# Performance work log

Hardware: AMD Instinct MI355X
Metric: run time of the kernel (lower is better)

Reference implementation:

```python
import math
import jax, jax.numpy as jnp
import numpy as np

B, C, HH, WW = 1, 256, 64, 64
NUM_HEADS = 8
GROUPS = 8
EPS = 1e-5


def setup_inputs() -> dict:
    key = jax.random.key(0)
    ks = jax.random.split(key, 5)
    x = jax.random.normal(ks[0], (B, C, HH, WW), dtype=jnp.float32)
    gn_gamma = jnp.ones((C,), dtype=jnp.float32)
    gn_beta = jnp.zeros((C,), dtype=jnp.float32)
    qkv_w = jax.random.normal(ks[1], (3 * C, C), dtype=jnp.float32) / math.sqrt(C)
    qkv_b = jax.random.normal(ks[2], (3 * C,), dtype=jnp.float32) * 0.02
    proj_w = jax.random.normal(ks[3], (C, C), dtype=jnp.float32) / math.sqrt(C)
    proj_b = jax.random.normal(ks[4], (C,), dtype=jnp.float32) * 0.02
    return {"x": x, "gn_gamma": gn_gamma, "gn_beta": gn_beta,
            "qkv_w": qkv_w, "qkv_b": qkv_b, "proj_w": proj_w, "proj_b": proj_b}


def reference(x, gn_gamma, gn_beta, qkv_w, qkv_b, proj_w, proj_b):
    b, c, h, w = x.shape
    t = h * w
    xf = x.reshape(b, c, t)
    # GroupNorm(8, C): normalize over (C/8 channels x T spatial) per group
    xg = xf.reshape(b, GROUPS, (c // GROUPS) * t)
    mean = xg.mean(axis=-1, keepdims=True)
    var = xg.var(axis=-1, keepdims=True)
    xn = ((xg - mean) * jax.lax.rsqrt(var + EPS)).reshape(b, c, t)
    xn = xn * gn_gamma[:, None] + gn_beta[:, None]
    # 1x1 Conv1d C -> 3C is a channel matmul
    qkv = jnp.einsum('oc,bct->bot', qkv_w, xn) + qkv_b[:, None]  # [b, 3C, t]
    nh = NUM_HEADS
    ch = c // nh
    q, k, v = jnp.split(qkv, 3, axis=1)  # each [b, C, t]
    q = q.reshape(b * nh, ch, t)
    k = k.reshape(b * nh, ch, t)
    v = v.reshape(b * nh, ch, t)
    scale = 1.0 / math.sqrt(math.sqrt(ch))
    weight = jnp.einsum('bct,bcs->bts', q * scale, k * scale)  # [b*nh, t, t]
    weight = jax.nn.softmax(weight.astype(jnp.float32), axis=-1).astype(qkv.dtype)
    a = jnp.einsum('bts,bcs->bct', weight, v).reshape(b, c, t)
    hout = jnp.einsum('oc,bct->bot', proj_w, a) + proj_b[:, None]
    return x + hout.reshape(b, c, h, w)
```

## Files before the change

### kernel.cpp

```cpp
#include <hip/hip_runtime.h>
#include <hip/hip_bf16.h>
#include <math.h>

#define C_DIM 256
#define T_DIM 4096
#define NHEADS 8
#define NGROUPS 8
#define NSPLIT 4
#define SRANGE (T_DIM / NSPLIT)
#define NT (SRANGE / 64)

typedef __attribute__((ext_vector_type(8))) short bf16x8;
typedef __attribute__((ext_vector_type(4))) float f32x4;

#if __has_builtin(__builtin_amdgcn_exp2f)
#define EXP2(x) __builtin_amdgcn_exp2f(x)
#else
#define EXP2(x) exp2f(x)
#endif

#define MFMA16(a, b, c) __builtin_amdgcn_mfma_f32_16x16x32_bf16(a, b, c, 0, 0, 0)

#define WS_PSUM 0
#define WS_PSQ  256
#define WS_QT_F   1024
#define WS_KT_F   (WS_QT_F + 524288)
#define WS_VB_F   (WS_KT_F + 524288)
#define WS_WQB_F  (WS_VB_F + 524288)
#define WS_WPB_F  (WS_WQB_F + 98304)
#define WS_OP_F   (WS_WPB_F + 32768)
#define WS_L_F    (WS_OP_F + NSPLIT * 256 * 4096 / 2)

#define QSCALE 0.2550348527f

__device__ __forceinline__ ushort f2bf(float f) {
  union { float f; unsigned u; } v; v.f = f;
  return (ushort)((v.u + 0x7fffu + ((v.u >> 16) & 1u)) >> 16);
}

__device__ __forceinline__ float bf2f(ushort u) {
  union { unsigned u; float f; } v; v.u = ((unsigned)u) << 16;
  return v.f;
}

__device__ __forceinline__ uint pk2(float a, float b) {
  __hip_bfloat162 h = __float22bfloat162_rn(make_float2(a, b));
  union { __hip_bfloat162 h; uint u; } c; c.h = h; return c.u;
}

__global__ __launch_bounds__(256) void prep(const float* __restrict__ x,
                                            const float* __restrict__ wq,
                                            const float* __restrict__ wp,
                                            float* __restrict__ ws,
                                            ushort* __restrict__ wqb,
                                            ushort* __restrict__ wpb) {
  const int i4 = (blockIdx.x * 256 + threadIdx.x) * 4;
  const int n1 = 768 * 256;
  if (i4 < n1) {
    float4 v = *(const float4*)(wq + i4);
    union { ushort us[4]; uint2 u; } pk;
    pk.us[0] = f2bf(v.x); pk.us[1] = f2bf(v.y); pk.us[2] = f2bf(v.z); pk.us[3] = f2bf(v.w);
    *(uint2*)(wqb + i4) = pk.u;
  } else {
    const int j = i4 - n1;
    float4 v = *(const float4*)(wp + j);
    union { ushort us[4]; uint2 u; } pk;
    pk.us[0] = f2bf(v.x); pk.us[1] = f2bf(v.y); pk.us[2] = f2bf(v.z); pk.us[3] = f2bf(v.w);
    *(uint2*)(wpb + j) = pk.u;
  }
  const int g = blockIdx.x >> 5;
  const int bx = blockIdx.x & 31;
  const size_t base = (size_t)g * 131072 + (size_t)bx * 4096;
  float s = 0.f, s2 = 0.f;
  for (int i = threadIdx.x; i < 4096; i += 256) {
    float v = x[base + i];
    s += v;
    s2 += v * v;
  }
#pragma unroll
  for (int mask = 1; mask <= 32; mask <<= 1) {
    s += __shfl_xor(s, mask, 64);
    s2 += __shfl_xor(s2, mask, 64);
  }
  __shared__ float red[8];
  const int wid = threadIdx.x >> 6;
  if ((threadIdx.x & 63) == 0) { red[wid] = s; red[4 + wid] = s2; }
  __syncthreads();
  if (threadIdx.x == 0) {
    ws[WS_PSUM + g * 32 + bx] = red[0] + red[1] + red[2] + red[3];
    ws[WS_PSQ + g * 32 + bx] = red[4] + red[5] + red[6] + red[7];
  }
}

__global__ __launch_bounds__(256) void qkv_mfma(const float* __restrict__ x,
                                                const float* __restrict__ gamma,
                                                const float* __restrict__ beta,
                                                const float* __restrict__ ws,
                                                const ushort* __restrict__ wqb,
                                                const float* __restrict__ bias,
                                                ushort* __restrict__ qt,
                                                ushort* __restrict__ kt,
                                                ushort* __restrict__ vb) {
  const int t0 = blockIdx.x * 16;
  const int oc = blockIdx.y;
  __shared__ ushort A[16 * 256];
  __shared__ float fg[256], fb[256];
  __shared__ float sm_stat[16];
  const int tid = threadIdx.x;
  {
    const int gg = tid >> 5, i = tid & 31;
    float s = ws[WS_PSUM + gg * 32 + i];
    float s2 = ws[WS_PSQ + gg * 32 + i];
#pragma unroll
    for (int mask = 1; mask <= 16; mask <<= 1) {
      s += __shfl_xor(s, mask, 32);
      s2 += __shfl_xor(s2, mask, 32);
    }
    if (i == 0) {
      const float inv_n = 1.0f / 131072.0f;
      float mean = s * inv_n;
      float var = s2 * inv_n - mean * mean;
      sm_stat[gg] = mean;
      sm_stat[8 + gg] = rsqrtf(var + 1e-5f);
    }
  }
  __syncthreads();
  {
    const int c = tid, gg = c >> 5;
    float fgv = gamma[c] * sm_stat[8 + gg];
    fg[c] = fgv; fb[c] = beta[c] - sm_stat[gg] * fgv;
  }
  __syncthreads();
#pragma unroll
  for (int p = 0; p < 4; ++p) {
    const int idx = p * 256 + tid;
    const int c = idx >> 2;
    const int tin = (idx & 3) * 4;
    float4 xv = *(const float4*)(x + (size_t)c * T_DIM + t0 + tin);
    const float fgc = fg[c], fbc = fb[c];
    float xn[4] = {fmaf(xv.x, fgc, fbc), fmaf(xv.y, fgc, fbc),
                   fmaf(xv.z, fgc, fbc), fmaf(xv.w, fgc, fbc)};
#pragma unroll
    for (int i = 0; i < 4; ++i) {
      const int t = tin + i;
      A[t * 256 + (c ^ ((t & 7) << 3))] = f2bf(xn[i]);
    }
  }
  __syncthreads();

  const int w = tid >> 6, lane = tid & 63, l15 = lane & 15, g = lane >> 4;
  const int o_loc = w * 64;
  f32x4 acc[4] = {};
  const ushort* wrow[4];
#pragma unroll
  for (int j = 0; j < 4; ++j)
    wrow[j] = wqb + (size_t)(oc * 256 + o_loc + j * 16 + l15) * 256;

  bf16x8 bc[4], bn[4];
#pragma unroll
  for (int j = 0; j < 4; ++j) bc[j] = *(const bf16x8*)(wrow[j] + 8 * g);

#pragma unroll
  for (int kk = 0; kk < 8; ++kk) {
    const bf16x8 af = *(const bf16x8*)(&A[l15 * 256 + ((kk * 32 + 8 * g) ^ ((l15 & 7) << 3))]);
    if (kk < 7) {
#pragma unroll
      for (int j = 0; j < 4; ++j) bn[j] = *(const bf16x8*)(wrow[j] + (kk + 1) * 32 + 8 * g);
    }
#pragma unroll
    for (int j = 0; j < 4; ++j)
      acc[j] = MFMA16(af, bc[j], acc[j]);
#pragma unroll
    for (int j = 0; j < 4; ++j) bc[j] = bn[j];
  }

  if (oc == 2) {
#pragma unroll
    for (int j = 0; j < 4; ++j) {
      const int o = o_loc + j * 16 + l15;
      const float bo = bias[512 + o];
      union { ushort us[4]; uint2 u; } pk;
#pragma unroll
      for (int r = 0; r < 4; ++r) pk.us[r] = f2bf(acc[j][r] + bo);
      *(uint2*)(vb + (size_t)o * T_DIM + t0 + 4 * g) = pk.u;
    }
  } else {
    const float scale = (oc == 0) ? QSCALE : 1.0f;
    __syncthreads();
#pragma unroll
    for (int j = 0; j < 4; ++j) {
      const int o = o_loc + j * 16 + l15;
      const float bo = bias[oc * 256 + o];
#pragma unroll
      for (int r = 0; r < 4; ++r) {
        const int t = 4 * g + r;
        A[t * 256 + (o ^ ((t & 7) << 3))] = f2bf((acc[j][r] + bo) * scale);
      }
    }
    __syncthreads();
    ushort* dst = (oc == 0) ? qt : kt;
    const int hh = tid >> 5;
    const int tt = (tid >> 1) & 15;
    const int d0 = (tid & 1) * 16;
    const int sw = (tt & 7) << 3;
    uint4 v0 = *(uint4*)&A[tt * 256 + ((hh * 32 + d0) ^ sw)];
    uint4 v1 = *(uint4*)&A[tt * 256 + ((hh * 32 + d0 + 8) ^ sw)];
    ushort* gp = dst + ((size_t)hh * T_DIM + t0 + tt) * 32 + d0;
    *(uint4*)gp = v0;
    *(uint4*)(gp + 8) = v1;
  }
}

__global__ __launch_bounds__(256, 4) void attn_fwd(const ushort* __restrict__ qt,
                                                   const ushort* __restrict__ kt,
                                                   const ushort* __restrict__ vb,
                                                   ushort* __restrict__ Op,
                                                   float* __restrict__ Lb) {
  const int bid = blockIdx.x;
  const int h = bid & 7;
  const int inner = bid >> 3;
  const int qb = inner & 31;
  const int z = inner >> 5;
  const int tid = threadIdx.x;
  const int w = tid >> 6, lane = tid & 63, l15 = lane & 15, g = lane >> 4;

  __shared__ ushort Klds[2][64 * 40];
  __shared__ ushort Vlds[2][32 * 72];

  const int t_a = qb * 128 + w * 16 + l15;
  const int t_b = t_a + 64;
  const bf16x8 qfa = *(const bf16x8*)(qt + ((size_t)(h * T_DIM + t_a) * 32 + 8 * g));
  const bf16x8 qfb = *(const bf16x8*)(qt + ((size_t)(h * T_DIM + t_b) * 32 + 8 * g));

  f32x4 Oa0 = {}, Oa1 = {}, Ob0 = {}, Ob1 = {};
  float la = 0.f, lb = 0.f;

  const int sbeg = z * SRANGE;
  const int p_row = tid >> 2;
  const int q5 = p_row & 31;
  const int sm_row = (p_row & 32) + 16 * ((q5 >> 2) & 1) + 4 * (q5 >> 3) + (q5 & 3);
  const ushort* kgp = kt + (size_t)h * T_DIM * 32 + (size_t)(sbeg + p_row) * 32 + (tid & 3) * 8;
  const ushort* vgp = vb + (size_t)(h * 32 + (tid >> 3)) * T_DIM + sbeg + (tid & 7) * 8;
  ushort* kw0 = &Klds[0][sm_row * 40 + (tid & 3) * 8];
  ushort* vw0 = &Vlds[0][(tid >> 3) * 72 + (tid & 7) * 8];
  {
    *(uint4*)kw0 = *(const uint4*)kgp;
    *(uint4*)vw0 = *(const uint4*)vgp;
  }
  uint4 kn = *(const uint4*)(kgp + 2048);
  uint4 vn = *(const uint4*)(vgp + 64);
  __syncthreads();

  int cur = 0;
  for (int t = 0; t < NT; ++t) {
    if (t + 1 < NT) {
      *(uint4*)(kw0 + (cur ^ 1) * (64 * 40)) = kn;
      *(uint4*)(vw0 + (cur ^ 1) * (32 * 72)) = vn;
      if (t + 2 < NT) {
        kn = *(const uint4*)(kgp + (size_t)(t + 2) * 2048);
        vn = *(const uint4*)(vgp + (t + 2) * 64);
      }
    }

    const ushort* kbase = &Klds[cur][0];
    const ushort* vbase = &Vlds[cur][0];
    const f32x4 z4 = {};
    const bf16x8 kf0 = *(const bf16x8*)(kbase + (0 * 16 + l15) * 40 + 8 * g);
    const bf16x8 kf1 = *(const bf16x8*)(kbase + (1 * 16 + l15) * 40 + 8 * g);
    const bf16x8 kf2 = *(const bf16x8*)(kbase + (2 * 16 + l15) * 40 + 8 * g);
    const bf16x8 kf3 = *(const bf16x8*)(kbase + (3 * 16 + l15) * 40 + 8 * g);
    __builtin_amdgcn_s_setprio(1);
    f32x4 sa0 = MFMA16(kf0, qfa, z4);
    f32x4 sa1 = MFMA16(kf1, qfa, z4);
    f32x4 sa2 = MFMA16(kf2, qfa, z4);
    f32x4 sa3 = MFMA16(kf3, qfa, z4);
    f32x4 sb0 = MFMA16(kf0, qfb, z4);
    f32x4 sb1 = MFMA16(kf1, qfb, z4);
    f32x4 sb2 = MFMA16(kf2, qfb, z4);
    f32x4 sb3 = MFMA16(kf3, qfb, z4);
    __builtin_amdgcn_s_setprio(0);

    const bf16x8 vf00 = *(const bf16x8*)(vbase + (l15) * 72 + 8 * g);
    const bf16x8 vf01 = *(const bf16x8*)(vbase + (l15) * 72 + 32 + 8 * g);
    const bf16x8 vf10 = *(const bf16x8*)(vbase + (16 + l15) * 72 + 8 * g);
    const bf16x8 vf11 = *(const bf16x8*)(vbase + (16 + l15) * 72 + 32 + 8 * g);

    union { uint u[4]; bf16x8 v; } fa0, fa1, fb0, fb1;
    {
      float p0, p1, p2, p3, p4, p5, p6, p7;
      p0 = EXP2(sa0[0]); p1 = EXP2(sa0[1]); p2 = EXP2(sa0[2]); p3 = EXP2(sa0[3]);
      p4 = EXP2(sa1[0]); p5 = EXP2(sa1[1]); p6 = EXP2(sa1[2]); p7 = EXP2(sa1[3]);
      la += ((p0 + p1) + (p2 + p3)) + ((p4 + p5) + (p6 + p7));
      fa0.u[0] = pk2(p0, p1); fa0.u[1] = pk2(p2, p3);
      fa0.u[2] = pk2(p4, p5); fa0.u[3] = pk2(p6, p7);
      p0 = EXP2(sa2[0]); p1 = EXP2(sa2[1]); p2 = EXP2(sa2[2]); p3 = EXP2(sa2[3]);
      p4 = EXP2(sa3[0]); p5 = EXP2(sa3[1]); p6 = EXP2(sa3[2]); p7 = EXP2(sa3[3]);
      la += ((p0 + p1) + (p2 + p3)) + ((p4 + p5) + (p6 + p7));
      fa1.u[0] = pk2(p0, p1); fa1.u[1] = pk2(p2, p3);
      fa1.u[2] = pk2(p4, p5); fa1.u[3] = pk2(p6, p7);
    }

    __builtin_amdgcn_s_setprio(1);
    Oa0 = MFMA16(vf00, fa0.v, Oa0);
    Oa0 = MFMA16(vf01, fa1.v, Oa0);
    Oa1 = MFMA16(vf10, fa0.v, Oa1);
    Oa1 = MFMA16(vf11, fa1.v, Oa1);
    __builtin_amdgcn_s_setprio(0);

    {
      float p0, p1, p2, p3, p4, p5, p6, p7;
      p0 = EXP2(sb0[0]); p1 = EXP2(sb0[1]); p2 = EXP2(sb0[2]); p3 = EXP2(sb0[3]);
      p4 = EXP2(sb1[0]); p5 = EXP2(sb1[1]); p6 = EXP2(sb1[2]); p7 = EXP2(sb1[3]);
      lb += ((p0 + p1) + (p2 + p3)) + ((p4 + p5) + (p6 + p7));
      fb0.u[0] = pk2(p0, p1); fb0.u[1] = pk2(p2, p3);
      fb0.u[2] = pk2(p4, p5); fb0.u[3] = pk2(p6, p7);
      p0 = EXP2(sb2[0]); p1 = EXP2(sb2[1]); p2 = EXP2(sb2[2]); p3 = EXP2(sb2[3]);
      p4 = EXP2(sb3[0]); p5 = EXP2(sb3[1]); p6 = EXP2(sb3[2]); p7 = EXP2(sb3[3]);
      lb += ((p0 + p1) + (p2 + p3)) + ((p4 + p5) + (p6 + p7));
      fb1.u[0] = pk2(p0, p1); fb1.u[1] = pk2(p2, p3);
      fb1.u[2] = pk2(p4, p5); fb1.u[3] = pk2(p6, p7);
    }

    __builtin_amdgcn_s_setprio(1);
    Ob0 = MFMA16(vf00, fb0.v, Ob0);
    Ob0 = MFMA16(vf01, fb1.v, Ob0);
    Ob1 = MFMA16(vf10, fb0.v, Ob1);
    Ob1 = MFMA16(vf11, fb1.v, Ob1);
    __builtin_amdgcn_s_setprio(0);

    __syncthreads();
    cur ^= 1;
  }

  ushort* opz = Op + (size_t)(z * NHEADS + h) * 32 * T_DIM;
#pragma unroll
  for (int r = 0; r < 4; ++r) {
    const int d0 = 4 * g + r;
    opz[(size_t)d0 * T_DIM + t_a]        = f2bf(Oa0[r]);
    opz[(size_t)(16 + d0) * T_DIM + t_a] = f2bf(Oa1[r]);
    opz[(size_t)d0 * T_DIM + t_b]        = f2bf(Ob0[r]);
    opz[(size_t)(16 + d0) * T_DIM + t_b] = f2bf(Ob1[r]);
  }
  la += __shfl_xor(la, 16, 64);
  la += __shfl_xor(la, 32, 64);
  lb += __shfl_xor(lb, 16, 64);
  lb += __shfl_xor(lb, 32, 64);
  if (g == 0) {
    Lb[(size_t)(z * NHEADS + h) * T_DIM + t_a] = la;
    Lb[(size_t)(z * NHEADS + h) * T_DIM + t_b] = lb;
  }
}

__global__ __launch_bounds__(256) void proj_mfma(const ushort* __restrict__ Op,
                                                 const float* __restrict__ Lb,
                                                 const ushort* __restrict__ wpb,
                                                 const float* __restrict__ bias,
                                                 const float* __restrict__ x,
                                                 float* __restrict__ out) {
  const int t0 = blockIdx.x * 16;
  __shared__ ushort A[16 * 256];
  __shared__ float rinv[128];
  const int tid = threadIdx.x;
  if (tid < 128) {
    const int h = tid >> 4, tt = tid & 15;
    float l = 0.f;
#pragma unroll
    for (int zz = 0; zz < NSPLIT; ++zz)
      l += Lb[(size_t)(zz * NHEADS + h) * T_DIM + t0 + tt];
    rinv[tid] = 1.0f / l;
  }
  __syncthreads();
#pragma unroll
  for (int pass = 0; pass < 4; ++pass) {
    const int c = pass * 64 + (tid >> 2);
    const int h = c >> 5;
    const int tin = (tid & 3) * 4;
    float a4[4] = {0.f, 0.f, 0.f, 0.f};
#pragma unroll
    for (int zz = 0; zz < NSPLIT; ++zz) {
      uint2 v = *(const uint2*)(Op + (size_t)(zz * 256 + c) * T_DIM + t0 + tin);
      const ushort* us = (const ushort*)&v;
#pragma unroll
      for (int i = 0; i < 4; ++i) a4[i] += bf2f(us[i]);
    }
#pragma unroll
    for (int i = 0; i < 4; ++i) {
      const int t = tin + i;
      A[t * 256 + (c ^ ((t & 7) << 3))] = f2bf(a4[i] * rinv[(h << 4) | t]);
    }
  }
  __syncthreads();

  const int w = tid >> 6, lane = tid & 63, l15 = lane & 15, g = lane >> 4;
  const int o0 = blockIdx.y * 128 + w * 32;
  f32x4 acc[2] = {};
  const ushort* wrow[2];
#pragma unroll
  for (int j = 0; j < 2; ++j)
    wrow[j] = wpb + (size_t)(o0 + 16 * j + l15) * 256;

#pragma unroll
  for (int kk = 0; kk < 8; ++kk) {
    const bf16x8 af = *(const bf16x8*)(&A[l15 * 256 + ((kk * 32 + 8 * g) ^ ((l15 & 7) << 3))]);
#pragma unroll
    for (int j = 0; j < 2; ++j) {
      const bf16x8 bfr = *(const bf16x8*)(wrow[j] + kk * 32 + 8 * g);
      acc[j] = MFMA16(af, bfr, acc[j]);
    }
  }

#pragma unroll
  for (int j = 0; j < 2; ++j) {
    const int o = o0 + 16 * j + l15;
    const float bo = bias[o];
    const size_t base = (size_t)o * T_DIM + t0 + 4 * g;
    const float4 xr = *(const float4*)(x + base);
    float4 ov;
    ov.x = acc[j][0] + bo + xr.x;
    ov.y = acc[j][1] + bo + xr.y;
    ov.z = acc[j][2] + bo + xr.z;
    ov.w = acc[j][3] + bo + xr.w;
    *(float4*)(out + base) = ov;
  }
}

extern "C" void kernel_launch(void* const* d_in, const int* in_sizes, int n_in,
                              void* d_out, int out_size, void* d_ws, size_t ws_size,
                              hipStream_t stream) {
  const float* x      = (const float*)d_in[0];
  const float* gamma  = (const float*)d_in[1];
  const float* beta   = (const float*)d_in[2];
  const float* qkv_w  = (const float*)d_in[3];
  const float* qkv_b  = (const float*)d_in[4];
  const float* proj_w = (const float*)d_in[5];
  const float* proj_b = (const float*)d_in[6];
  float* out = (float*)d_out;
  float* ws  = (float*)d_ws;

  ushort* qt  = (ushort*)(ws + WS_QT_F);
  ushort* kt  = (ushort*)(ws + WS_KT_F);
  ushort* vb  = (ushort*)(ws + WS_VB_F);
  ushort* wqb = (ushort*)(ws + WS_WQB_F);
  ushort* wpb = (ushort*)(ws + WS_WPB_F);
  ushort* Op  = (ushort*)(ws + WS_OP_F);
  float*  Lb  = ws + WS_L_F;

  prep<<<256, 256, 0, stream>>>(x, qkv_w, proj_w, ws, wqb, wpb);
  qkv_mfma<<<dim3(256, 3), 256, 0, stream>>>(x, gamma, beta, ws, wqb, qkv_b, qt, kt, vb);
  attn_fwd<<<NHEADS * 32 * NSPLIT, 256, 0, stream>>>(qt, kt, vb, Op, Lb);
  proj_mfma<<<dim3(256, 2), 256, 0, stream>>>(Op, Lb, wpb, proj_b, x, out);
}
```

Before: 68.05 us.

## Double KV split count, store partial outputs token-major, merge proj blocks

Raises the attention key-split factor from 4 to 8, giving twice as many attention blocks for better CU occupancy, each covering a shorter key range. Partial outputs are now stored token-major ([z][t][c]) with vectorized 8-byte stores instead of scattered 2-byte channel-major stores. The projection kernel reads them with 16-byte loads and computes all 256 output channels per block, so the split reduction runs once instead of twice across two y-blocks. The cost is twice the partial-output traffic and a longer reduction over splits in proj.

Measured after the change: 67.35 us. About the same (-1.0%).

```diff
diff --git a/kernel.cpp b/kernel.cpp
--- a/kernel.cpp
+++ b/kernel.cpp
@@ -6,7 +6,7 @@
 #define T_DIM 4096
 #define NHEADS 8
 #define NGROUPS 8
-#define NSPLIT 4
+#define NSPLIT 8
 #define SRANGE (T_DIM / NSPLIT)
 #define NT (SRANGE / 64)
 
@@ -29,7 +29,7 @@
 #define WS_WQB_F  (WS_VB_F + 524288)
 #define WS_WPB_F  (WS_WQB_F + 98304)
 #define WS_OP_F   (WS_WPB_F + 32768)
-#define WS_L_F    (WS_OP_F + NSPLIT * 256 * 4096 / 2)
+#define WS_L_F    (WS_OP_F + NSPLIT * T_DIM * 256 / 2)
 
 #define QSCALE 0.2550348527f
 
@@ -332,14 +332,17 @@
     cur ^= 1;
   }
 
-  ushort* opz = Op + (size_t)(z * NHEADS + h) * 32 * T_DIM;
-#pragma unroll
-  for (int r = 0; r < 4; ++r) {
-    const int d0 = 4 * g + r;
-    opz[(size_t)d0 * T_DIM + t_a]        = f2bf(Oa0[r]);
-    opz[(size_t)(16 + d0) * T_DIM + t_a] = f2bf(Oa1[r]);
-    opz[(size_t)d0 * T_DIM + t_b]        = f2bf(Ob0[r]);
-    opz[(size_t)(16 + d0) * T_DIM + t_b] = f2bf(Ob1[r]);
+  ushort* opz = Op + (size_t)z * T_DIM * 256;
+  {
+    union { ushort us[4]; uint2 u; } p0, p1;
+#pragma unroll
+    for (int r = 0; r < 4; ++r) { p0.us[r] = f2bf(Oa0[r]); p1.us[r] = f2bf(Oa1[r]); }
+    *(uint2*)(opz + (size_t)t_a * 256 + h * 32 + 4 * g) = p0.u;
+    *(uint2*)(opz + (size_t)t_a * 256 + h * 32 + 16 + 4 * g) = p1.u;
+#pragma unroll
+    for (int r = 0; r < 4; ++r) { p0.us[r] = f2bf(Ob0[r]); p1.us[r] = f2bf(Ob1[r]); }
+    *(uint2*)(opz + (size_t)t_b * 256 + h * 32 + 4 * g) = p0.u;
+    *(uint2*)(opz + (size_t)t_b * 256 + h * 32 + 16 + 4 * g) = p1.u;
   }
   la += __shfl_xor(la, 16, 64);
   la += __shfl_xor(la, 32, 64);
@@ -371,46 +374,45 @@
   }
   __syncthreads();
 #pragma unroll
-  for (int pass = 0; pass < 4; ++pass) {
-    const int c = pass * 64 + (tid >> 2);
-    const int h = c >> 5;
-    const int tin = (tid & 3) * 4;
-    float a4[4] = {0.f, 0.f, 0.f, 0.f};
+  for (int p = 0; p < 2; ++p) {
+    const int t = p * 8 + (tid >> 5);
+    const int c0 = (tid & 31) * 8;
+    float a8[8] = {0.f, 0.f, 0.f, 0.f, 0.f, 0.f, 0.f, 0.f};
 #pragma unroll
     for (int zz = 0; zz < NSPLIT; ++zz) {
-      uint2 v = *(const uint2*)(Op + (size_t)(zz * 256 + c) * T_DIM + t0 + tin);
+      uint4 v = *(const uint4*)(Op + ((size_t)zz * T_DIM + t0 + t) * 256 + c0);
       const ushort* us = (const ushort*)&v;
 #pragma unroll
-      for (int i = 0; i < 4; ++i) a4[i] += bf2f(us[i]);
-    }
-#pragma unroll
-    for (int i = 0; i < 4; ++i) {
-      const int t = tin + i;
-      A[t * 256 + (c ^ ((t & 7) << 3))] = f2bf(a4[i] * rinv[(h << 4) | t]);
-    }
+      for (int i = 0; i < 8; ++i) a8[i] += bf2f(us[i]);
+    }
+    const float ri = rinv[(c0 >> 5) * 16 + t];
+    union { ushort us[8]; uint4 u; } pk;
+#pragma unroll
+    for (int i = 0; i < 8; ++i) pk.us[i] = f2bf(a8[i] * ri);
+    *(uint4*)&A[t * 256 + (c0 ^ ((t & 7) << 3))] = pk.u;
   }
   __syncthreads();
 
   const int w = tid >> 6, lane = tid & 63, l15 = lane & 15, g = lane >> 4;
-  const int o0 = blockIdx.y * 128 + w * 32;
-  f32x4 acc[2] = {};
-  const ushort* wrow[2];
-#pragma unroll
-  for (int j = 0; j < 2; ++j)
+  const int o0 = w * 64;
+  f32x4 acc[4] = {};
+  const ushort* wrow[4];
+#pragma unroll
+  for (int j = 0; j < 4; ++j)
     wrow[j] = wpb + (size_t)(o0 + 16 * j + l15) * 256;
 
 #pragma unroll
   for (int kk = 0; kk < 8; ++kk) {
     const bf16x8 af = *(const bf16x8*)(&A[l15 * 256 + ((kk * 32 + 8 * g) ^ ((l15 & 7) << 3))]);
 #pragma unroll
-    for (int j = 0; j < 2; ++j) {
+    for (int j = 0; j < 4; ++j) {
       const bf16x8 bfr = *(const bf16x8*)(wrow[j] + kk * 32 + 8 * g);
       acc[j] = MFMA16(af, bfr, acc[j]);
     }
   }
 
 #pragma unroll
-  for (int j = 0; j < 2; ++j) {
+  for (int j = 0; j < 4; ++j) {
     const int o = o0 + 16 * j + l15;
     const float bo = bias[o];
     const size_t base = (size_t)o * T_DIM + t0 + 4 * g;
@@ -448,5 +450,5 @@
   prep<<<256, 256, 0, stream>>>(x, qkv_w, proj_w, ws, wqb, wpb);
   qkv_mfma<<<dim3(256, 3), 256, 0, stream>>>(x, gamma, beta, ws, wqb, qkv_b, qt, kt, vb);
   attn_fwd<<<NHEADS * 32 * NSPLIT, 256, 0, stream>>>(qt, kt, vb, Op, Lb);
-  proj_mfma<<<dim3(256, 2), 256, 0, stream>>>(Op, Lb, wpb, proj_b, x, out);
-}
+  proj_mfma<<<256, 256, 0, stream>>>(Op, Lb, wpb, proj_b, x, out);
+}
```
